# Optimization experiments

Measured on AMD Instinct MI355X. Metric: run time of the kernel, lower is better.

## Reference

```python
import jax, jax.numpy as jnp
import numpy as np
import math

HEADS = 2
DH = 64
INNER = HEADS * DH  # 128
TOPK = 128
ALPHA = 10.0
N_FREQ = 8  # feature_dim // (2*input_dim) = 64 // 8
OMEGAS = jnp.logspace(1.0, math.log10(128.0), N_FREQ)           # sigma_q = 128
OMEGAS_L = [jnp.logspace(1.0, math.log10(s), N_FREQ) for s in (128.0, 32.0)]
LAYER_NUM = 2


def calc_gamma(grid, omegas):
    # grid: (Q, 4) -> (Q, 4*2*n_freq)
    arg = jnp.pi * grid[:, :, None] * omegas[None, None, :]      # (Q,4,n)
    g = jnp.concatenate([jnp.sin(arg), jnp.cos(arg)], axis=-1)   # (Q,4,2n)
    return g.reshape(grid.shape[0], -1)


def setup_inputs() -> dict:
    key = jax.random.key(0)
    ks = jax.random.split(key, 20)
    B, Q, L, HD, FD, OD = 2, 4096, 1024, 256, 64, 1

    def w(k, shape, fan_in):
        return jax.random.normal(k, shape, dtype=jnp.float32) * (1.0 / np.sqrt(fan_in))

    inp = {
        'x': jax.random.uniform(ks[0], (B, Q, 4), dtype=jnp.float32),
        'tokens': jax.random.normal(ks[1], (B, L, HD), dtype=jnp.float32),
        'query_W': w(ks[2], (FD, HD), FD),
        'query_b': jnp.zeros((HD,), jnp.float32),
        'q_W': w(ks[3], (HD, INNER), HD),
        'kv_W': w(ks[4], (HD, 2 * INNER), HD),
        'out_W': w(ks[5], (INNER, HD), INNER),
        'out_b': jnp.zeros((HD,), jnp.float32),
        'band_W': w(ks[6], (LAYER_NUM, FD, HD), FD),
        'band_b': jnp.zeros((LAYER_NUM, HD), jnp.float32),
        'mod_W': w(ks[7], (LAYER_NUM, HD, HD), HD),
        'mod_b': jnp.zeros((LAYER_NUM, HD), jnp.float32),
        'hv_W': w(ks[8], (LAYER_NUM - 1, HD, HD), HD),
        'hv_b': jnp.zeros((LAYER_NUM - 1, HD), jnp.float32),
        'outl_W': w(ks[9], (LAYER_NUM, HD, OD), HD),
        'outl_b': jnp.zeros((LAYER_NUM, OD), jnp.float32),
        'gD': 8, 'gH': 8, 'gW': 8, 'gT': 8,
    }
    return inp


def reference(x, tokens, query_W, query_b, q_W, kv_W, out_W, out_b,
              band_W, band_b, mod_W, mod_b, hv_W, hv_b, outl_W, outl_b,
              gD, gH, gW, gT):
    B, Q, _ = x.shape
    L = tokens.shape[1]
    grid = x[0]  # (Q, 4) — torch code uses x[0] for all batches

    # --- patch index + approximate relative distances -> sparse attn indices ---
    z_i = (grid[:, 0] * gD).astype(jnp.int32)
    y_i = (grid[:, 1] * gH).astype(jnp.int32)
    x_i = (grid[:, 2] * gW).astype(jnp.int32)
    t_i = (grid[:, 3] * gT).astype(jnp.int32)
    idx = ((t_i * gD + z_i) * gH + y_i) * gW + x_i               # (Q,)
    N = gD * gH * gW * gT
    t = idx / N                                                  # (Q,) float
    tok_pos = (jnp.arange(L, dtype=jnp.float32) + 0.5) / L       # (L,)
    bias = ALPHA * (t[:, None] - tok_pos[None, :]) ** 2          # (Q, L)
    # top-k SMALLEST distances (identical across batch, compute once)
    _, attn_idx = jax.lax.top_k(-bias, TOPK)                     # (Q, k)

    # --- query features ---
    gamma_q = calc_gamma(grid, OMEGAS)                           # (Q, 64)
    x_q = jax.nn.relu(gamma_q @ query_W + query_b)               # (Q, 256)
    x_q = jnp.broadcast_to(x_q[None], (B, Q, x_q.shape[-1]))

    # --- sparse shared-token cross attention ---
    scale = DH ** -0.5
    q = (x_q @ q_W).reshape(B, Q, HEADS, DH)                     # (B,Q,H,Dh)
    kv = tokens @ kv_W                                           # (B,L,2*inner)
    k_full, v_full = kv[..., :INNER], kv[..., INNER:]            # (B,L,inner)
    k_sp = k_full[:, attn_idx, :].reshape(B, Q, TOPK, HEADS, DH)  # (B,Q,k,H,Dh)
    v_sp = v_full[:, attn_idx, :].reshape(B, Q, TOPK, HEADS, DH)
    sim = jnp.einsum('bqhd,bqkhd->bhqk', q, k_sp) * scale        # (B,H,Q,k)
    attn = jax.nn.softmax(sim, axis=-1)
    o = jnp.einsum('bhqk,bqkhd->bqhd', attn, v_sp).reshape(B, Q, INNER)
    modulation = o @ out_W + out_b                               # (B,Q,256)

    # --- per-band modulation ---
    mods = []
    for l in range(LAYER_NUM):
        gamma_l = calc_gamma(grid, OMEGAS_L[l])                  # (Q, 64)
        h_l = jax.nn.relu(gamma_l @ band_W[l] + band_b[l])       # (Q, 256)
        m_l = jax.nn.relu(h_l[None] + modulation @ mod_W[l] + mod_b[l])
        mods.append(m_l)

    h_v = [mods[0]]
    for i in range(LAYER_NUM - 1):
        h_v.append(jax.nn.relu((mods[i + 1] + h_v[i]) @ hv_W[i] + hv_b[i]))

    out = sum(h_v[i] @ outl_W[i] + outl_b[i] for i in range(LAYER_NUM))
    return out  # (B, Q, output_dim)
```

## Files before the change

kernel.cpp:

```cpp
#include <hip/hip_runtime.h>
#include <math.h>

#define BN     2
#define QN     4096
#define LN     1024
#define TOPKN  128
#define PI_F   3.14159265358979323846f

#define K_OM0  0.3642064529893673
#define K_OM1  0.1661644014008115

#define NCMAX  320
#define PFP    328

typedef __attribute__((ext_vector_type(8))) short  s16x8;
typedef __attribute__((ext_vector_type(4))) float  f32x4;

__device__ __forceinline__ unsigned short f2bf(float f) {
    unsigned int u = __float_as_uint(f);
    u = (u + 0x7FFFu + ((u >> 16) & 1u)) >> 16;
    return (unsigned short)u;
}

struct KvSmem {
    unsigned short tok_bf[16 * 264];
    unsigned short stage[256 * 40];
    float ktile[128][20];
};
struct QSmem {
    float sh_x[128];
    unsigned short gam_bf[32 * 72];
    unsigned short xq_bf[32 * 264];
    unsigned short stage[256 * 40];
};
struct TrSmem { float tile[32][33]; };
struct SortSmem { int hist[1024]; int psum[256]; };
union PrepSmem { KvSmem kv; QSmem q; TrSmem tr; SortSmem so; };

__global__ __launch_bounds__(256) void prep_kernel(
    const float* __restrict__ tokens, const float* __restrict__ kv_W,
    const float* __restrict__ x, const float* __restrict__ query_W,
    const float* __restrict__ query_b, const float* __restrict__ q_W,
    const float* __restrict__ outW, const float* __restrict__ bandW,
    const float* __restrict__ modW, const float* __restrict__ hvW,
    const int* __restrict__ gDp, const int* __restrict__ gHp,
    const int* __restrict__ gWp, const int* __restrict__ gTp,
    float* __restrict__ qall, unsigned short* __restrict__ kbf,
    unsigned short* __restrict__ vtbf,
    unsigned short* __restrict__ outT, unsigned short* __restrict__ bandT,
    unsigned short* __restrict__ modT, unsigned short* __restrict__ hvT,
    int* __restrict__ perm, int* __restrict__ ssort)
{
    __shared__ __align__(16) PrepSmem sm;
    const int bid = blockIdx.x, t = threadIdx.x;

    if (bid < 128) {
        int l0 = bid * 16;
        int b = l0 >> 10, lloc = l0 & 1023;
        #pragma unroll
        for (int i = 0; i < 16; i++)
            sm.kv.tok_bf[i * 264 + t] = f2bf(tokens[(size_t)(l0 + i) * 256 + t]);
        int w = t >> 6, lane = t & 63, quad = lane >> 4, l16 = lane & 15;
        int n0 = w * 64;
        f32x4 acc[4];
        #pragma unroll
        for (int s = 0; s < 4; s++) acc[s] = (f32x4){0.f, 0.f, 0.f, 0.f};
        for (int kc = 0; kc < 8; kc++) {
            __syncthreads();
            #pragma unroll
            for (int i = 0; i < 32; i++)
                sm.kv.stage[t * 40 + i] = f2bf(kv_W[(size_t)(kc * 32 + i) * 256 + t]);
            __syncthreads();
            s16x8 a = *(const s16x8*)&sm.kv.tok_bf[l16 * 264 + kc * 32 + quad * 8];
            #pragma unroll
            for (int sub = 0; sub < 4; sub++) {
                s16x8 bfr = *(const s16x8*)&sm.kv.stage[(n0 + sub * 16 + l16) * 40 + quad * 8];
                acc[sub] = __builtin_amdgcn_mfma_f32_16x16x32_bf16(a, bfr, acc[sub], 0, 0, 0);
            }
        }
        if (w < 2) {
            #pragma unroll
            for (int sub = 0; sub < 4; sub++)
                #pragma unroll
                for (int r = 0; r < 4; r++)
                    kbf[(size_t)(l0 + quad * 4 + r) * 128 + n0 + sub * 16 + l16] =
                        f2bf(acc[sub][r]);
        } else {
            #pragma unroll
            for (int sub = 0; sub < 4; sub++)
                #pragma unroll
                for (int r = 0; r < 4; r++)
                    sm.kv.ktile[(n0 - 128) + sub * 16 + l16][quad * 4 + r] = acc[sub][r];
        }
        __syncthreads();
        {
            int col = t >> 1, half = t & 1;
            s16x8 pk;
            #pragma unroll
            for (int j = 0; j < 8; j++)
                pk[j] = (short)f2bf(sm.kv.ktile[col][half * 8 + j]);
            *(s16x8*)&vtbf[(size_t)(b * 128 + col) * 1024 + lloc + half * 8] = pk;
        }
    } else if (bid < 256) {
        int p0 = (bid - 128) * 32;
        if (t < 128) sm.q.sh_x[t] = x[p0 * 4 + t];
        __syncthreads();
        {
            int e0 = t * 8;
            int g = e0 >> 6;
            #pragma unroll
            for (int j = 0; j < 8; j++) {
                int f = (e0 + j) & 63;
                int c = f >> 4, jj = f & 15, oi = jj & 7;
                float om = (float)(10.0 * exp((double)oi * K_OM0));
                float arg = PI_F * sm.q.sh_x[g * 4 + c] * om;
                sm.q.gam_bf[g * 72 + f] = f2bf((jj < 8) ? sinf(arg) : cosf(arg));
            }
        }
        int w = t >> 6, lane = t & 63, quad = lane >> 4, l16 = lane & 15;
        int m0 = (w >> 1) * 16;
        {
            int n0a = (w & 1) * 128;
            f32x4 acc[8];
            #pragma unroll
            for (int s = 0; s < 8; s++) acc[s] = (f32x4){0.f, 0.f, 0.f, 0.f};
            for (int kc = 0; kc < 2; kc++) {
                __syncthreads();
                #pragma unroll
                for (int i = 0; i < 32; i++)
                    sm.q.stage[t * 40 + i] = f2bf(query_W[(size_t)(kc * 32 + i) * 256 + t]);
                __syncthreads();
                s16x8 a = *(const s16x8*)&sm.q.gam_bf[(m0 + l16) * 72 + kc * 32 + quad * 8];
                #pragma unroll
                for (int sub = 0; sub < 8; sub++) {
                    s16x8 bfr = *(const s16x8*)&sm.q.stage[(n0a + sub * 16 + l16) * 40 + quad * 8];
                    acc[sub] = __builtin_amdgcn_mfma_f32_16x16x32_bf16(a, bfr, acc[sub], 0, 0, 0);
                }
            }
            #pragma unroll
            for (int sub = 0; sub < 8; sub++) {
                int col = n0a + sub * 16 + l16;
                float bias = query_b[col];
                #pragma unroll
                for (int r = 0; r < 4; r++)
                    sm.q.xq_bf[(m0 + quad * 4 + r) * 264 + col] = f2bf(fmaxf(acc[sub][r] + bias, 0.f));
            }
        }
        {
            int n0b = (w & 1) * 64;
            f32x4 acc2[4];
            #pragma unroll
            for (int s = 0; s < 4; s++) acc2[s] = (f32x4){0.f, 0.f, 0.f, 0.f};
            for (int kc = 0; kc < 8; kc++) {
                __syncthreads();
                #pragma unroll
                for (int i = 0; i < 16; i++) {
                    int e = i * 256 + t;
                    int k = e >> 7, n = e & 127;
                    sm.q.stage[n * 40 + k] = f2bf(q_W[(size_t)(kc * 32 + k) * 128 + n]);
                }
                __syncthreads();
                s16x8 a = *(const s16x8*)&sm.q.xq_bf[(m0 + l16) * 264 + kc * 32 + quad * 8];
                #pragma unroll
                for (int sub = 0; sub < 4; sub++) {
                    s16x8 bfr = *(const s16x8*)&sm.q.stage[(n0b + sub * 16 + l16) * 40 + quad * 8];
                    acc2[sub] = __builtin_amdgcn_mfma_f32_16x16x32_bf16(a, bfr, acc2[sub], 0, 0, 0);
                }
            }
            #pragma unroll
            for (int sub = 0; sub < 4; sub++)
                #pragma unroll
                for (int r = 0; r < 4; r++)
                    qall[(size_t)(p0 + m0 + quad * 4 + r) * 128 + n0b + sub * 16 + l16] = acc2[sub][r];
        }
    } else if (bid < 512) {
        int bid2 = bid - 256;
        const float* src; unsigned short* dst; int K, N, lt;
        if      (bid2 < 32)  { src = outW;  dst = outT;  K = 128; N = 256; lt = bid2; }
        else if (bid2 < 64)  { src = bandW; dst = bandT; K = 128; N = 256; lt = bid2 - 32; }
        else if (bid2 < 192) { src = modW;  dst = modT;  K = 512; N = 256; lt = bid2 - 64; }
        else                 { src = hvW;   dst = hvT;   K = 256; N = 256; lt = bid2 - 192; }
        int tk = K >> 5;
        int ktile = lt % tk, nt = lt / tk;
        int k0 = ktile * 32, n0 = nt * 32;
        int tx = t & 31, ty = t >> 5;
        #pragma unroll
        for (int r = 0; r < 4; r++)
            sm.tr.tile[ty + 8 * r][tx] = src[(size_t)(k0 + ty + 8 * r) * N + n0 + tx];
        __syncthreads();
        #pragma unroll
        for (int r = 0; r < 4; r++)
            dst[(size_t)(n0 + ty + 8 * r) * K + k0 + tx] = f2bf(sm.tr.tile[tx][ty + 8 * r]);
    } else {
        int gD = gDp[0], gH = gHp[0], gW = gWp[0], gT = gTp[0];
        int Ng = gD * gH * gW * gT;
        #pragma unroll
        for (int i = 0; i < 4; i++) sm.so.hist[t + 256 * i] = 0;
        __syncthreads();
        int sarr[16];
        #pragma unroll
        for (int i = 0; i < 16; i++) {
            int q = i * 256 + t;
            float4 xv = *(const float4*)&x[q * 4];
            int zi = (int)(xv.x * (float)gD);
            int yi = (int)(xv.y * (float)gH);
            int xi = (int)(xv.z * (float)gW);
            int ti = (int)(xv.w * (float)gT);
            int idx = ((ti * gD + zi) * gH + yi) * gW + xi;
            float tt = (float)idx / (float)Ng;
            int s = (int)ceilf(tt * (float)LN - ((float)(TOPKN / 2) + 0.5f));
            s = min(max(s, 0), LN - TOPKN);
            sarr[i] = s;
            atomicAdd(&sm.so.hist[s], 1);
        }
        __syncthreads();
        int sum4 = sm.so.hist[4 * t] + sm.so.hist[4 * t + 1]
                 + sm.so.hist[4 * t + 2] + sm.so.hist[4 * t + 3];
        sm.so.psum[t] = sum4;
        __syncthreads();
        for (int off = 1; off < 256; off <<= 1) {
            int v = (t >= off) ? sm.so.psum[t - off] : 0;
            __syncthreads();
            sm.so.psum[t] += v;
            __syncthreads();
        }
        int base = sm.so.psum[t] - sum4;
        int b0 = sm.so.hist[4 * t], b1 = sm.so.hist[4 * t + 1], b2 = sm.so.hist[4 * t + 2];
        sm.so.hist[4 * t] = base;
        sm.so.hist[4 * t + 1] = base + b0;
        sm.so.hist[4 * t + 2] = base + b0 + b1;
        sm.so.hist[4 * t + 3] = base + b0 + b1 + b2;
        __syncthreads();
        #pragma unroll
        for (int i = 0; i < 16; i++) {
            int q = i * 256 + t;
            int pos = atomicAdd(&sm.so.hist[sarr[i]], 1);
            perm[pos] = q;
            ssort[pos] = sarr[i];
        }
    }
}

__global__ __launch_bounds__(1024, 8) void fused_kernel(
    const float* __restrict__ x,
    const unsigned short* __restrict__ kbf, const unsigned short* __restrict__ vtbf,
    const float* __restrict__ qall,
    const int* __restrict__ perm, const int* __restrict__ ssort,
    const unsigned short* __restrict__ outT, const float* __restrict__ out_b,
    const unsigned short* __restrict__ bandT, const float* __restrict__ band_b,
    const unsigned short* __restrict__ modT, const float* __restrict__ mod_b,
    const unsigned short* __restrict__ hvT, const float* __restrict__ hv_b,
    const float* __restrict__ outl_W, const float* __restrict__ outl_b,
    float* __restrict__ out)
{
    const int bid = blockIdx.x;
    const int b   = bid >> 8;
    const int sp0 = (bid & 255) * 16;
    const int t   = threadIdx.x;
    const int wid = t >> 6, lane = t & 63;
    const int quad = lane >> 4, l16 = lane & 15;

    __shared__ __align__(16) unsigned short q_bf[16 * 136];
    __shared__ __align__(16) unsigned short gam_lds[32 * 72];
    __shared__ __align__(16) unsigned short P_bf[32 * PFP];
    __shared__ __align__(16) unsigned char regionA[PFP * 16 * 4];
    __shared__ __align__(16) unsigned short o_lds[16 * 136];
    __shared__ float fin[256];
    __shared__ float sh_xc[64];
    __shared__ int sh_pq[16], sh_s[16];

    float* P_f32 = (float*)regionA;
    float* o_part = (float*)regionA;
    unsigned short* modu_lds = (unsigned short*)regionA;
    unsigned short* s01_lds  = (unsigned short*)(regionA + 16 * 264 * 2);

    if (t < 16) { sh_pq[t] = perm[sp0 + t]; sh_s[t] = ssort[sp0 + t]; }
    __syncthreads();

    {
        int m = t >> 6, d = (t & 63) * 2;
        float2 qv = *(const float2*)&qall[(size_t)sh_pq[m] * 128 + d];
        unsigned int pk = (unsigned int)f2bf(qv.x) | ((unsigned int)f2bf(qv.y) << 16);
        *(unsigned int*)&q_bf[m * 136 + d] = pk;
    }
    if (t < 64) sh_xc[t] = x[(size_t)sh_pq[t >> 2] * 4 + (t & 3)];
    __syncthreads();

    #pragma unroll
    for (int j = 0; j < 2; j++) {
        int e = t * 2 + j;
        int l = e >> 10, g = (e >> 6) & 15, f = e & 63;
        int c = f >> 4, jj = f & 15, oi = jj & 7;
        float om = (float)(10.0 * exp((double)oi * (l ? K_OM1 : K_OM0)));
        float arg = PI_F * sh_xc[g * 4 + c] * om;
        gam_lds[(l * 16 + g) * 72 + f] = f2bf((jj < 8) ? sinf(arg) : cosf(arg));
    }

    const int u0    = sh_s[0] & ~7;
    const int ncols = min((sh_s[15] + 128 - u0 + 31) & ~31, NCMAX);
    const int nsub  = ncols >> 4;
    const int nkc   = ncols >> 5;

    #pragma unroll
    for (int h = 0; h < 2; h++) {
        s16x8 aq0 = *(const s16x8*)&q_bf[l16 * 136 + h * 64 + quad * 8];
        s16x8 aq1 = *(const s16x8*)&q_bf[l16 * 136 + h * 64 + 32 + quad * 8];
        for (int sub = wid; sub < nsub; sub += 16) {
            f32x4 acc = (f32x4){0.f, 0.f, 0.f, 0.f};
            size_t krow = (size_t)(b * 1024 + u0 + sub * 16 + l16) * 128 + h * 64 + quad * 8;
            s16x8 b0 = *(const s16x8*)&kbf[krow];
            s16x8 b1 = *(const s16x8*)&kbf[krow + 32];
            acc = __builtin_amdgcn_mfma_f32_16x16x32_bf16(aq0, b0, acc, 0, 0, 0);
            acc = __builtin_amdgcn_mfma_f32_16x16x32_bf16(aq1, b1, acc, 0, 0, 0);
            #pragma unroll
            for (int r = 0; r < 4; r++)
                P_f32[(quad * 4 + r) * PFP + sub * 16 + l16] = acc[r];
        }
        __syncthreads();
        {
            int g = wid;
            int sg = sh_s[g];
            float vals[5]; int ok[5];
            float mx = -1e30f;
            #pragma unroll
            for (int i = 0; i < 5; i++) {
                int c = lane + 64 * i;
                float v = P_f32[g * PFP + c] * 0.125f;
                int key = u0 + c;
                int o2 = (c < ncols) && (key >= sg) && (key < sg + 128);
                vals[i] = v; ok[i] = o2;
                if (o2) mx = fmaxf(mx, v);
            }
            #pragma unroll
            for (int off = 1; off < 64; off <<= 1) mx = fmaxf(mx, __shfl_xor(mx, off));
            float sum = 0.f, e5[5];
            #pragma unroll
            for (int i = 0; i < 5; i++) {
                float e = ok[i] ? expf(vals[i] - mx) : 0.f;
                e5[i] = e; sum += e;
            }
            #pragma unroll
            for (int off = 1; off < 64; off <<= 1) sum += __shfl_xor(sum, off);
            float inv = 1.f / sum;
            #pragma unroll
            for (int i = 0; i < 5; i++) {
                int c = lane + 64 * i;
                if (c < ncols) P_bf[(h * 16 + g) * PFP + c] = f2bf(e5[i] * inv);
            }
        }
        __syncthreads();
    }

    {
        int n0 = (wid & 7) * 16;
        int hh = n0 >> 6;
        int khalf = wid >> 3;
        int nk2 = (nkc + 1) >> 1;
        int k0 = khalf ? nk2 : 0;
        int k1 = khalf ? nkc : nk2;
        f32x4 acc = (f32x4){0.f, 0.f, 0.f, 0.f};
        for (int kc = k0; kc < k1; kc++) {
            s16x8 a = *(const s16x8*)&P_bf[(hh * 16 + l16) * PFP + kc * 32 + quad * 8];
            int koff = u0 + kc * 32 + quad * 8;
            koff = min(koff, 1016);
            s16x8 bfr = *(const s16x8*)&vtbf[(size_t)(b * 128 + n0 + l16) * 1024 + koff];
            acc = __builtin_amdgcn_mfma_f32_16x16x32_bf16(a, bfr, acc, 0, 0, 0);
        }
        #pragma unroll
        for (int r = 0; r < 4; r++)
            o_part[(khalf * 16 + quad * 4 + r) * 128 + n0 + l16] = acc[r];
    }
    __syncthreads();

    {
        int m = t >> 6, j2 = (t & 63) * 2;
        float v0 = o_part[m * 128 + j2]     + o_part[(16 + m) * 128 + j2];
        float v1 = o_part[m * 128 + j2 + 1] + o_part[(16 + m) * 128 + j2 + 1];
        unsigned int pk = (unsigned int)f2bf(v0) | ((unsigned int)f2bf(v1) << 16);
        *(unsigned int*)&o_lds[m * 136 + j2] = pk;
    }
    __syncthreads();

    const int n0 = wid * 16;
    float m0f[4];

    {
        f32x4 acc = (f32x4){0.f, 0.f, 0.f, 0.f};
        #pragma unroll
        for (int kc = 0; kc < 4; kc++) {
            s16x8 a = *(const s16x8*)&o_lds[l16 * 136 + kc * 32 + quad * 8];
            s16x8 bfr = *(const s16x8*)&outT[(size_t)(n0 + l16) * 128 + kc * 32 + quad * 8];
            acc = __builtin_amdgcn_mfma_f32_16x16x32_bf16(a, bfr, acc, 0, 0, 0);
        }
        int col = n0 + l16;
        float bias = out_b[col];
        #pragma unroll
        for (int r = 0; r < 4; r++)
            modu_lds[(quad * 4 + r) * 264 + col] = f2bf(acc[r] + bias);
    }
    __syncthreads();

    #pragma unroll
    for (int l = 0; l < 2; l++) {
        f32x4 acc1 = (f32x4){0.f, 0.f, 0.f, 0.f};
        f32x4 acc2 = (f32x4){0.f, 0.f, 0.f, 0.f};
        #pragma unroll
        for (int kc = 0; kc < 2; kc++) {
            s16x8 a = *(const s16x8*)&gam_lds[(l * 16 + l16) * 72 + kc * 32 + quad * 8];
            s16x8 bfr = *(const s16x8*)&bandT[(size_t)(n0 + l16) * 128 + l * 64 + kc * 32 + quad * 8];
            acc1 = __builtin_amdgcn_mfma_f32_16x16x32_bf16(a, bfr, acc1, 0, 0, 0);
        }
        #pragma unroll
        for (int kc = 0; kc < 8; kc++) {
            s16x8 a = *(const s16x8*)&modu_lds[l16 * 264 + kc * 32 + quad * 8];
            s16x8 bfr = *(const s16x8*)&modT[(size_t)(n0 + l16) * 512 + l * 256 + kc * 32 + quad * 8];
            acc2 = __builtin_amdgcn_mfma_f32_16x16x32_bf16(a, bfr, acc2, 0, 0, 0);
        }
        int col = n0 + l16;
        float bb = band_b[l * 256 + col];
        float mb = mod_b[l * 256 + col];
        #pragma unroll
        for (int r = 0; r < 4; r++) {
            float hval = fmaxf(acc1[r] + bb, 0.f);
            float mval = fmaxf(hval + acc2[r] + mb, 0.f);
            if (l == 0) m0f[r] = mval;
            else s01_lds[(quad * 4 + r) * 264 + col] = f2bf(m0f[r] + mval);
        }
    }
    __syncthreads();

    {
        f32x4 acc = (f32x4){0.f, 0.f, 0.f, 0.f};
        #pragma unroll
        for (int kc = 0; kc < 8; kc++) {
            s16x8 a = *(const s16x8*)&s01_lds[l16 * 264 + kc * 32 + quad * 8];
            s16x8 bfr = *(const s16x8*)&hvT[(size_t)(n0 + l16) * 256 + kc * 32 + quad * 8];
            acc = __builtin_amdgcn_mfma_f32_16x16x32_bf16(a, bfr, acc, 0, 0, 0);
        }
        int col = n0 + l16;
        float w0 = outl_W[col], w1 = outl_W[256 + col], hb = hv_b[col];
        #pragma unroll
        for (int r = 0; r < 4; r++) {
            float hvv = fmaxf(acc[r] + hb, 0.f);
            float pv = m0f[r] * w0 + hvv * w1;
            #pragma unroll
            for (int off = 1; off < 16; off <<= 1) pv += __shfl_xor(pv, off);
            if (l16 == 0) fin[wid * 16 + quad * 4 + r] = pv;
        }
    }
    __syncthreads();
    if (t < 16) {
        float s2 = outl_b[0] + outl_b[1];
        #pragma unroll
        for (int w = 0; w < 16; w++) s2 += fin[w * 16 + t];
        out[(size_t)b * QN + sh_pq[t]] = s2;
    }
}

extern "C" void kernel_launch(void* const* d_in, const int* in_sizes, int n_in,
                              void* d_out, int out_size, void* d_ws, size_t ws_size,
                              hipStream_t stream)
{
    const float* x       = (const float*)d_in[0];
    const float* tokens  = (const float*)d_in[1];
    const float* query_W = (const float*)d_in[2];
    const float* query_b = (const float*)d_in[3];
    const float* q_W     = (const float*)d_in[4];
    const float* kv_W    = (const float*)d_in[5];
    const float* out_W   = (const float*)d_in[6];
    const float* out_b   = (const float*)d_in[7];
    const float* band_W  = (const float*)d_in[8];
    const float* band_b  = (const float*)d_in[9];
    const float* mod_W   = (const float*)d_in[10];
    const float* mod_b   = (const float*)d_in[11];
    const float* hv_W    = (const float*)d_in[12];
    const float* hv_b    = (const float*)d_in[13];
    const float* outl_W  = (const float*)d_in[14];
    const float* outl_b  = (const float*)d_in[15];
    const int*   gD      = (const int*)d_in[16];
    const int*   gH      = (const int*)d_in[17];
    const int*   gW      = (const int*)d_in[18];
    const int*   gT      = (const int*)d_in[19];

    float* ws   = (float*)d_ws;
    float* qall = ws;
    unsigned short* wb = (unsigned short*)(ws + 524288);
    unsigned short* kbf   = wb;
    unsigned short* vtbf  = wb + 262144;
    unsigned short* outT  = wb + 524288;
    unsigned short* bandT = wb + 557056;
    unsigned short* modT  = wb + 589824;
    unsigned short* hvT   = wb + 720896;
    int* perm  = (int*)(wb + 786432);
    int* ssort = perm + 4096;
    float* out = (float*)d_out;

    prep_kernel<<<513, 256, 0, stream>>>(tokens, kv_W, x, query_W, query_b, q_W,
                                         out_W, band_W, mod_W, hv_W,
                                         gD, gH, gW, gT,
                                         qall, kbf, vtbf, outT, bandT, modT, hvT,
                                         perm, ssort);
    fused_kernel<<<512, 1024, 0, stream>>>(x, kbf, vtbf, qall, perm, ssort,
        outT, out_b, bandT, band_b, modT, mod_b, hvT, hv_b,
        outl_W, outl_b, out);
}
```

Before: 146.3 us.

## Widen prep kernel to 1024-thread blocks with larger per-block tiles

Moves the prep kernel from 256-thread to 1024-thread blocks. KV projection blocks now handle 32 rows each instead of 16, with 16 waves each owning a 16x32 output tile. Q-projection waves take smaller column slices, transpose blocks cover one 32x32 tile per block, and the sort uses a flat 1024-entry scan. This cuts the block count and spreads each block's staging loads over more threads, at the cost of more barriers per block and lower MFMA work per wave.

New measurement: 145.8 us. Within noise of the previous version (-0.3%).

```diff
diff --git a/kernel.cpp b/kernel.cpp
--- a/kernel.cpp
+++ b/kernel.cpp
@@ -14,30 +14,23 @@
 #define PFP    328
 
 typedef __attribute__((ext_vector_type(8))) short  s16x8;
+typedef __attribute__((ext_vector_type(4))) short  s16x4;
 typedef __attribute__((ext_vector_type(4))) float  f32x4;
-
-__device__ __forceinline__ unsigned short f2bf(float f) {
+typedef unsigned short u16;
+
+__device__ __forceinline__ u16 f2bf(float f) {
     unsigned int u = __float_as_uint(f);
     u = (u + 0x7FFFu + ((u >> 16) & 1u)) >> 16;
-    return (unsigned short)u;
+    return (u16)u;
 }
 
-struct KvSmem {
-    unsigned short tok_bf[16 * 264];
-    unsigned short stage[256 * 40];
-    float ktile[128][20];
-};
-struct QSmem {
-    float sh_x[128];
-    unsigned short gam_bf[32 * 72];
-    unsigned short xq_bf[32 * 264];
-    unsigned short stage[256 * 40];
-};
-struct TrSmem { float tile[32][33]; };
-struct SortSmem { int hist[1024]; int psum[256]; };
-union PrepSmem { KvSmem kv; QSmem q; TrSmem tr; SortSmem so; };
-
-__global__ __launch_bounds__(256) void prep_kernel(
+struct KvS { u16 tok[32 * 264]; u16 stage[256 * 40]; float vtile[128][40]; };
+struct QS  { float shx[128]; u16 gam[32 * 72]; u16 xq[32 * 264]; u16 stage[256 * 40]; };
+struct TrS { float tile[32][33]; };
+struct SoS { int hist[1024]; int cur[1024]; };
+union PrepS { KvS kv; QS q; TrS tr; SoS so; };
+
+__global__ __launch_bounds__(1024) void prep_kernel(
     const float* __restrict__ tokens, const float* __restrict__ kv_W,
     const float* __restrict__ x, const float* __restrict__ query_W,
     const float* __restrict__ query_b, const float* __restrict__ q_W,
@@ -45,137 +38,132 @@
     const float* __restrict__ modW, const float* __restrict__ hvW,
     const int* __restrict__ gDp, const int* __restrict__ gHp,
     const int* __restrict__ gWp, const int* __restrict__ gTp,
-    float* __restrict__ qall, unsigned short* __restrict__ kbf,
-    unsigned short* __restrict__ vtbf,
-    unsigned short* __restrict__ outT, unsigned short* __restrict__ bandT,
-    unsigned short* __restrict__ modT, unsigned short* __restrict__ hvT,
+    float* __restrict__ qall, u16* __restrict__ kbf, u16* __restrict__ vtbf,
+    u16* __restrict__ outT, u16* __restrict__ bandT,
+    u16* __restrict__ modT, u16* __restrict__ hvT,
     int* __restrict__ perm, int* __restrict__ ssort)
 {
-    __shared__ __align__(16) PrepSmem sm;
-    const int bid = blockIdx.x, t = threadIdx.x;
-
-    if (bid < 128) {
-        int l0 = bid * 16;
+    __shared__ __align__(16) PrepS sm;
+    const int bid = blockIdx.x;
+    const int t   = threadIdx.x;
+    const int wid = t >> 6, lane = t & 63;
+    const int quad = lane >> 4, l16 = lane & 15;
+
+    if (bid < 64) {
+        int l0 = bid * 32;
         int b = l0 >> 10, lloc = l0 & 1023;
         #pragma unroll
-        for (int i = 0; i < 16; i++)
-            sm.kv.tok_bf[i * 264 + t] = f2bf(tokens[(size_t)(l0 + i) * 256 + t]);
-        int w = t >> 6, lane = t & 63, quad = lane >> 4, l16 = lane & 15;
-        int n0 = w * 64;
-        f32x4 acc[4];
-        #pragma unroll
-        for (int s = 0; s < 4; s++) acc[s] = (f32x4){0.f, 0.f, 0.f, 0.f};
+        for (int i = 0; i < 8; i++) {
+            int idx = i * 1024 + t; int row = idx >> 8, col = idx & 255;
+            sm.kv.tok[row * 264 + col] = f2bf(tokens[(size_t)(l0 + row) * 256 + col]);
+        }
+        int m0 = (wid & 1) * 16;
+        int c0 = (wid >> 1) * 32;
+        f32x4 acc[2];
+        acc[0] = (f32x4){0.f, 0.f, 0.f, 0.f};
+        acc[1] = (f32x4){0.f, 0.f, 0.f, 0.f};
         for (int kc = 0; kc < 8; kc++) {
             __syncthreads();
             #pragma unroll
-            for (int i = 0; i < 32; i++)
-                sm.kv.stage[t * 40 + i] = f2bf(kv_W[(size_t)(kc * 32 + i) * 256 + t]);
+            for (int i = 0; i < 8; i++) {
+                int idx = i * 1024 + t; int k = idx >> 8, n = idx & 255;
+                sm.kv.stage[n * 40 + k] = f2bf(kv_W[(size_t)(kc * 32 + k) * 256 + n]);
+            }
             __syncthreads();
-            s16x8 a = *(const s16x8*)&sm.kv.tok_bf[l16 * 264 + kc * 32 + quad * 8];
-            #pragma unroll
-            for (int sub = 0; sub < 4; sub++) {
-                s16x8 bfr = *(const s16x8*)&sm.kv.stage[(n0 + sub * 16 + l16) * 40 + quad * 8];
+            s16x8 a = *(const s16x8*)&sm.kv.tok[(m0 + l16) * 264 + kc * 32 + quad * 8];
+            #pragma unroll
+            for (int sub = 0; sub < 2; sub++) {
+                s16x8 bfr = *(const s16x8*)&sm.kv.stage[(c0 + sub * 16 + l16) * 40 + quad * 8];
                 acc[sub] = __builtin_amdgcn_mfma_f32_16x16x32_bf16(a, bfr, acc[sub], 0, 0, 0);
             }
         }
-        if (w < 2) {
-            #pragma unroll
-            for (int sub = 0; sub < 4; sub++)
+        #pragma unroll
+        for (int sub = 0; sub < 2; sub++) {
+            int col = c0 + sub * 16 + l16;
+            if (col < 128) {
                 #pragma unroll
                 for (int r = 0; r < 4; r++)
-                    kbf[(size_t)(l0 + quad * 4 + r) * 128 + n0 + sub * 16 + l16] =
-                        f2bf(acc[sub][r]);
-        } else {
-            #pragma unroll
-            for (int sub = 0; sub < 4; sub++)
+                    kbf[(size_t)(l0 + m0 + quad * 4 + r) * 128 + col] = f2bf(acc[sub][r]);
+            } else {
                 #pragma unroll
                 for (int r = 0; r < 4; r++)
-                    sm.kv.ktile[(n0 - 128) + sub * 16 + l16][quad * 4 + r] = acc[sub][r];
+                    sm.kv.vtile[col - 128][m0 + quad * 4 + r] = acc[sub][r];
+            }
         }
         __syncthreads();
         {
-            int col = t >> 1, half = t & 1;
-            s16x8 pk;
-            #pragma unroll
-            for (int j = 0; j < 8; j++)
-                pk[j] = (short)f2bf(sm.kv.ktile[col][half * 8 + j]);
-            *(s16x8*)&vtbf[(size_t)(b * 128 + col) * 1024 + lloc + half * 8] = pk;
-        }
-    } else if (bid < 256) {
-        int p0 = (bid - 128) * 32;
-        if (t < 128) sm.q.sh_x[t] = x[p0 * 4 + t];
-        __syncthreads();
+            int col = t >> 3, rg = (t & 7) * 4;
+            float4 v4 = *(const float4*)&sm.kv.vtile[col][rg];
+            s16x4 pk;
+            pk[0] = (short)f2bf(v4.x); pk[1] = (short)f2bf(v4.y);
+            pk[2] = (short)f2bf(v4.z); pk[3] = (short)f2bf(v4.w);
+            *(s16x4*)&vtbf[(size_t)(b * 128 + col) * 1024 + lloc + rg] = pk;
+        }
+    } else if (bid < 192) {
+        int p0 = (bid - 64) * 32;
+        if (t < 128) sm.q.shx[t] = x[p0 * 4 + t];
+        __syncthreads();
+        #pragma unroll
+        for (int j = 0; j < 2; j++) {
+            int e = t * 2 + j;
+            int g = e >> 6, f = e & 63;
+            int c = f >> 4, jj = f & 15, oi = jj & 7;
+            float om = (float)(10.0 * exp((double)oi * K_OM0));
+            float arg = PI_F * sm.q.shx[g * 4 + c] * om;
+            sm.q.gam[g * 72 + f] = f2bf((jj < 8) ? sinf(arg) : cosf(arg));
+        }
+        int m0 = (wid & 1) * 16;
         {
-            int e0 = t * 8;
-            int g = e0 >> 6;
-            #pragma unroll
-            for (int j = 0; j < 8; j++) {
-                int f = (e0 + j) & 63;
-                int c = f >> 4, jj = f & 15, oi = jj & 7;
-                float om = (float)(10.0 * exp((double)oi * K_OM0));
-                float arg = PI_F * sm.q.sh_x[g * 4 + c] * om;
-                sm.q.gam_bf[g * 72 + f] = f2bf((jj < 8) ? sinf(arg) : cosf(arg));
-            }
-        }
-        int w = t >> 6, lane = t & 63, quad = lane >> 4, l16 = lane & 15;
-        int m0 = (w >> 1) * 16;
-        {
-            int n0a = (w & 1) * 128;
-            f32x4 acc[8];
-            #pragma unroll
-            for (int s = 0; s < 8; s++) acc[s] = (f32x4){0.f, 0.f, 0.f, 0.f};
+            int c0 = (wid >> 1) * 32;
+            f32x4 acc[2];
+            acc[0] = (f32x4){0.f, 0.f, 0.f, 0.f};
+            acc[1] = (f32x4){0.f, 0.f, 0.f, 0.f};
             for (int kc = 0; kc < 2; kc++) {
                 __syncthreads();
                 #pragma unroll
-                for (int i = 0; i < 32; i++)
-                    sm.q.stage[t * 40 + i] = f2bf(query_W[(size_t)(kc * 32 + i) * 256 + t]);
+                for (int i = 0; i < 8; i++) {
+                    int idx = i * 1024 + t; int k = idx >> 8, n = idx & 255;
+                    sm.q.stage[n * 40 + k] = f2bf(query_W[(size_t)(kc * 32 + k) * 256 + n]);
+                }
                 __syncthreads();
-                s16x8 a = *(const s16x8*)&sm.q.gam_bf[(m0 + l16) * 72 + kc * 32 + quad * 8];
-                #pragma unroll
-                for (int sub = 0; sub < 8; sub++) {
-                    s16x8 bfr = *(const s16x8*)&sm.q.stage[(n0a + sub * 16 + l16) * 40 + quad * 8];
+                s16x8 a = *(const s16x8*)&sm.q.gam[(m0 + l16) * 72 + kc * 32 + quad * 8];
+                #pragma unroll
+                for (int sub = 0; sub < 2; sub++) {
+                    s16x8 bfr = *(const s16x8*)&sm.q.stage[(c0 + sub * 16 + l16) * 40 + quad * 8];
                     acc[sub] = __builtin_amdgcn_mfma_f32_16x16x32_bf16(a, bfr, acc[sub], 0, 0, 0);
                 }
             }
             #pragma unroll
-            for (int sub = 0; sub < 8; sub++) {
-                int col = n0a + sub * 16 + l16;
+            for (int sub = 0; sub < 2; sub++) {
+                int col = c0 + sub * 16 + l16;
                 float bias = query_b[col];
                 #pragma unroll
                 for (int r = 0; r < 4; r++)
-                    sm.q.xq_bf[(m0 + quad * 4 + r) * 264 + col] = f2bf(fmaxf(acc[sub][r] + bias, 0.f));
+                    sm.q.xq[(m0 + quad * 4 + r) * 264 + col] = f2bf(fmaxf(acc[sub][r] + bias, 0.f));
             }
         }
         {
-            int n0b = (w & 1) * 64;
-            f32x4 acc2[4];
-            #pragma unroll
-            for (int s = 0; s < 4; s++) acc2[s] = (f32x4){0.f, 0.f, 0.f, 0.f};
+            int n0q = (wid >> 1) * 16;
+            f32x4 acc2 = (f32x4){0.f, 0.f, 0.f, 0.f};
             for (int kc = 0; kc < 8; kc++) {
                 __syncthreads();
                 #pragma unroll
-                for (int i = 0; i < 16; i++) {
-                    int e = i * 256 + t;
-                    int k = e >> 7, n = e & 127;
+                for (int i = 0; i < 4; i++) {
+                    int idx = i * 1024 + t; int k = idx >> 7, n = idx & 127;
                     sm.q.stage[n * 40 + k] = f2bf(q_W[(size_t)(kc * 32 + k) * 128 + n]);
                 }
                 __syncthreads();
-                s16x8 a = *(const s16x8*)&sm.q.xq_bf[(m0 + l16) * 264 + kc * 32 + quad * 8];
-                #pragma unroll
-                for (int sub = 0; sub < 4; sub++) {
-                    s16x8 bfr = *(const s16x8*)&sm.q.stage[(n0b + sub * 16 + l16) * 40 + quad * 8];
-                    acc2[sub] = __builtin_amdgcn_mfma_f32_16x16x32_bf16(a, bfr, acc2[sub], 0, 0, 0);
-                }
-            }
-            #pragma unroll
-            for (int sub = 0; sub < 4; sub++)
-                #pragma unroll
-                for (int r = 0; r < 4; r++)
-                    qall[(size_t)(p0 + m0 + quad * 4 + r) * 128 + n0b + sub * 16 + l16] = acc2[sub][r];
-        }
-    } else if (bid < 512) {
-        int bid2 = bid - 256;
-        const float* src; unsigned short* dst; int K, N, lt;
+                s16x8 a = *(const s16x8*)&sm.q.xq[(m0 + l16) * 264 + kc * 32 + quad * 8];
+                s16x8 bfr = *(const s16x8*)&sm.q.stage[(n0q + l16) * 40 + quad * 8];
+                acc2 = __builtin_amdgcn_mfma_f32_16x16x32_bf16(a, bfr, acc2, 0, 0, 0);
+            }
+            #pragma unroll
+            for (int r = 0; r < 4; r++)
+                qall[(size_t)(p0 + m0 + quad * 4 + r) * 128 + n0q + l16] = acc2[r];
+        }
+    } else if (bid < 448) {
+        int bid2 = bid - 192;
+        const float* src; u16* dst; int K, N, lt;
         if      (bid2 < 32)  { src = outW;  dst = outT;  K = 128; N = 256; lt = bid2; }
         else if (bid2 < 64)  { src = bandW; dst = bandT; K = 128; N = 256; lt = bid2 - 32; }
         else if (bid2 < 192) { src = modW;  dst = modT;  K = 512; N = 256; lt = bid2 - 64; }
@@ -183,24 +171,19 @@
         int tk = K >> 5;
         int ktile = lt % tk, nt = lt / tk;
         int k0 = ktile * 32, n0 = nt * 32;
-        int tx = t & 31, ty = t >> 5;
-        #pragma unroll
-        for (int r = 0; r < 4; r++)
-            sm.tr.tile[ty + 8 * r][tx] = src[(size_t)(k0 + ty + 8 * r) * N + n0 + tx];
-        __syncthreads();
-        #pragma unroll
-        for (int r = 0; r < 4; r++)
-            dst[(size_t)(n0 + ty + 8 * r) * K + k0 + tx] = f2bf(sm.tr.tile[tx][ty + 8 * r]);
+        int tx = t & 31, ty = (t >> 5) & 31;
+        sm.tr.tile[ty][tx] = src[(size_t)(k0 + ty) * N + n0 + tx];
+        __syncthreads();
+        dst[(size_t)(n0 + ty) * K + k0 + tx] = f2bf(sm.tr.tile[tx][ty]);
     } else {
         int gD = gDp[0], gH = gHp[0], gW = gWp[0], gT = gTp[0];
         int Ng = gD * gH * gW * gT;
-        #pragma unroll
-        for (int i = 0; i < 4; i++) sm.so.hist[t + 256 * i] = 0;
-        __syncthreads();
-        int sarr[16];
-        #pragma unroll
-        for (int i = 0; i < 16; i++) {
-            int q = i * 256 + t;
+        sm.so.hist[t] = 0;
+        __syncthreads();
+        int sarr[4];
+        #pragma unroll
+        for (int i = 0; i < 4; i++) {
+            int q = i * 1024 + t;
             float4 xv = *(const float4*)&x[q * 4];
             int zi = (int)(xv.x * (float)gD);
             int yi = (int)(xv.y * (float)gH);
@@ -214,26 +197,22 @@
             atomicAdd(&sm.so.hist[s], 1);
         }
         __syncthreads();
-        int sum4 = sm.so.hist[4 * t] + sm.so.hist[4 * t + 1]
-                 + sm.so.hist[4 * t + 2] + sm.so.hist[4 * t + 3];
-        sm.so.psum[t] = sum4;
-        __syncthreads();
-        for (int off = 1; off < 256; off <<= 1) {
-            int v = (t >= off) ? sm.so.psum[t - off] : 0;
+        int cnt = sm.so.hist[t];
+        sm.so.cur[t] = cnt;
+        __syncthreads();
+        for (int off = 1; off < 1024; off <<= 1) {
+            int u = (t >= off) ? sm.so.cur[t - off] : 0;
             __syncthreads();
-            sm.so.psum[t] += v;
+            sm.so.cur[t] += u;
             __syncthreads();
         }
-        int base = sm.so.psum[t] - sum4;
-        int b0 = sm.so.hist[4 * t], b1 = sm.so.hist[4 * t + 1], b2 = sm.so.hist[4 * t + 2];
-        sm.so.hist[4 * t] = base;
-        sm.so.hist[4 * t + 1] = base + b0;
-        sm.so.hist[4 * t + 2] = base + b0 + b1;
-        sm.so.hist[4 * t + 3] = base + b0 + b1 + b2;
-        __syncthreads();
-        #pragma unroll
-        for (int i = 0; i < 16; i++) {
-            int q = i * 256 + t;
+        int excl = sm.so.cur[t] - cnt;
+        __syncthreads();
+        sm.so.hist[t] = excl;
+        __syncthreads();
+        #pragma unroll
+        for (int i = 0; i < 4; i++) {
+            int q = i * 1024 + t;
             int pos = atomicAdd(&sm.so.hist[sarr[i]], 1);
             perm[pos] = q;
             ssort[pos] = sarr[i];
@@ -243,13 +222,13 @@
 
 __global__ __launch_bounds__(1024, 8) void fused_kernel(
     const float* __restrict__ x,
-    const unsigned short* __restrict__ kbf, const unsigned short* __restrict__ vtbf,
+    const u16* __restrict__ kbf, const u16* __restrict__ vtbf,
     const float* __restrict__ qall,
     const int* __restrict__ perm, const int* __restrict__ ssort,
-    const unsigned short* __restrict__ outT, const float* __restrict__ out_b,
-    const unsigned short* __restrict__ bandT, const float* __restrict__ band_b,
-    const unsigned short* __restrict__ modT, const float* __restrict__ mod_b,
-    const unsigned short* __restrict__ hvT, const float* __restrict__ hv_b,
+    const u16* __restrict__ outT, const float* __restrict__ out_b,
+    const u16* __restrict__ bandT, const float* __restrict__ band_b,
+    const u16* __restrict__ modT, const float* __restrict__ mod_b,
+    const u16* __restrict__ hvT, const float* __restrict__ hv_b,
     const float* __restrict__ outl_W, const float* __restrict__ outl_b,
     float* __restrict__ out)
 {
@@ -260,19 +239,19 @@
     const int wid = t >> 6, lane = t & 63;
     const int quad = lane >> 4, l16 = lane & 15;
 
-    __shared__ __align__(16) unsigned short q_bf[16 * 136];
-    __shared__ __align__(16) unsigned short gam_lds[32 * 72];
-    __shared__ __align__(16) unsigned short P_bf[32 * PFP];
+    __shared__ __align__(16) u16 q_bf[16 * 136];
+    __shared__ __align__(16) u16 gam_lds[32 * 72];
+    __shared__ __align__(16) u16 P_bf[32 * PFP];
     __shared__ __align__(16) unsigned char regionA[PFP * 16 * 4];
-    __shared__ __align__(16) unsigned short o_lds[16 * 136];
+    __shared__ __align__(16) u16 o_lds[16 * 136];
     __shared__ float fin[256];
     __shared__ float sh_xc[64];
     __shared__ int sh_pq[16], sh_s[16];
 
     float* P_f32 = (float*)regionA;
     float* o_part = (float*)regionA;
-    unsigned short* modu_lds = (unsigned short*)regionA;
-    unsigned short* s01_lds  = (unsigned short*)(regionA + 16 * 264 * 2);
+    u16* modu_lds = (u16*)regionA;
+    u16* s01_lds  = (u16*)(regionA + 16 * 264 * 2);
 
     if (t < 16) { sh_pq[t] = perm[sp0 + t]; sh_s[t] = ssort[sp0 + t]; }
     __syncthreads();
@@ -484,22 +463,22 @@
 
     float* ws   = (float*)d_ws;
     float* qall = ws;
-    unsigned short* wb = (unsigned short*)(ws + 524288);
-    unsigned short* kbf   = wb;
-    unsigned short* vtbf  = wb + 262144;
-    unsigned short* outT  = wb + 524288;
-    unsigned short* bandT = wb + 557056;
-    unsigned short* modT  = wb + 589824;
-    unsigned short* hvT   = wb + 720896;
+    u16* wb = (u16*)(ws + 524288);
+    u16* kbf   = wb;
+    u16* vtbf  = wb + 262144;
+    u16* outT  = wb + 524288;
+    u16* bandT = wb + 557056;
+    u16* modT  = wb + 589824;
+    u16* hvT   = wb + 720896;
     int* perm  = (int*)(wb + 786432);
     int* ssort = perm + 4096;
     float* out = (float*)d_out;
 
-    prep_kernel<<<513, 256, 0, stream>>>(tokens, kv_W, x, query_W, query_b, q_W,
-                                         out_W, band_W, mod_W, hv_W,
-                                         gD, gH, gW, gT,
-                                         qall, kbf, vtbf, outT, bandT, modT, hvT,
-                                         perm, ssort);
+    prep_kernel<<<449, 1024, 0, stream>>>(tokens, kv_W, x, query_W, query_b, q_W,
+                                          out_W, band_W, mod_W, hv_W,
+                                          gD, gH, gW, gT,
+                                          qall, kbf, vtbf, outT, bandT, modT, hvT,
+                                          perm, ssort);
     fused_kernel<<<512, 1024, 0, stream>>>(x, kbf, vtbf, qall, perm, ssort,
         outT, out_b, bandT, band_b, modT, mod_b, hvT, hv_b,
         outl_W, outl_b, out);
```
